# Optimization experiments

Hardware: AMD Instinct MI355X
Metric: run time of the kernel (lower is better)

## Reference

```python
import jax, jax.numpy as jnp
import numpy as np

QC = 12          # effective quantum channels (quantum_channels//4*4)
G = 3            # number of 4-channel quantum groups
DIM = 128
NGROUPS_GN = 8
NUM_LAYER = 1

# PauliZ sign table: wire 0 is the most-significant qubit (PennyLane default.qubit)
_SIGNS = np.array([[1.0 - 2.0 * ((k >> (3 - w)) & 1) for w in range(4)]
                   for k in range(16)], dtype=np.float32)


def _apply_rx(state, phi, w):
    # state: [B,2,2,2,2] complex64; phi: [B]; RX = cos(p/2) I - i sin(p/2) X
    c = jnp.cos(0.5 * phi).astype(jnp.complex64)
    s = (-1j) * jnp.sin(0.5 * phi).astype(jnp.complex64)
    U = jnp.stack([jnp.stack([c, s], -1), jnp.stack([s, c], -1)], -2)  # [B,2,2]
    st = jnp.moveaxis(state, 1 + w, -1)
    st = jnp.einsum('bij,b...j->b...i', U, st)
    return jnp.moveaxis(st, -1, 1 + w)


def _apply_cnot(state, c, t):
    st = jnp.moveaxis(state, (1 + c, 1 + t), (-2, -1))
    st = jnp.concatenate([st[..., 0:1, :], st[..., 1:2, ::-1]], axis=-2)
    return jnp.moveaxis(st, (-2, -1), (1 + c, 1 + t))


def _circuit(x4, theta):
    # AngleEmbedding(RX) + NUM_LAYER x Basic_ansatz; x4: [B,4], theta: [4*NUM_LAYER]
    B = x4.shape[0]
    state = jnp.zeros((B, 2, 2, 2, 2), jnp.complex64).at[:, 0, 0, 0, 0].set(1.0)
    for w in range(4):
        state = _apply_rx(state, x4[:, w], w)
    for l in range(NUM_LAYER):
        th = theta[4 * l:4 * (l + 1)]
        for w in range(4):
            state = _apply_rx(state, jnp.broadcast_to(th[w], (B,)), w)
        for c in range(3):
            state = _apply_cnot(state, c, c + 1)
        state = _apply_cnot(state, 3, 0)
    probs = jnp.abs(state.reshape(B, 16)) ** 2
    return probs @ jnp.asarray(_SIGNS)  # [B,4] PauliZ expvals


def _quantum_block(x_q, qparams):
    # x_q: [B,H,W,QC]; pool spatially, run per-group circuit, broadcast back
    B, H, W, Cq = x_q.shape
    pooled = jnp.mean(x_q, axis=(1, 2)).reshape(B, Cq // 4, 4)
    y = jax.vmap(_circuit, in_axes=(1, 0), out_axes=1)(pooled, qparams)  # [B,G,4]
    y = y.reshape(B, 1, 1, Cq)
    return jnp.broadcast_to(y, (B, H, W, Cq))


def _ws_conv(x, kernel, bias):
    eps = 1e-5  # fp32 branch of WeightStandardizedConv
    mean = jnp.mean(kernel, axis=(0, 1, 2), keepdims=True)
    var = jnp.var(kernel, axis=(0, 1, 2), keepdims=True)
    k = (kernel - mean) / jnp.sqrt(var + eps)
    y = jax.lax.conv_general_dilated(x, k, (1, 1), ((1, 1), (1, 1)),
                                     dimension_numbers=('NHWC', 'HWIO', 'NHWC'))
    return y + bias


def _group_norm(x, scale, bias, groups=NGROUPS_GN, eps=1e-6):
    B, H, W, C = x.shape
    xg = x.reshape(B, H, W, groups, C // groups)
    mu = jnp.mean(xg, axis=(1, 2, 4), keepdims=True)
    var = jnp.var(xg, axis=(1, 2, 4), keepdims=True)
    xn = ((xg - mu) / jnp.sqrt(var + eps)).reshape(B, H, W, C)
    return xn * scale + bias


def setup_inputs() -> dict:
    key = jax.random.key(0)
    ks = jax.random.split(key, 8)
    B, H, W, C, T = 16, 64, 64, DIM, 512
    cc = DIM - QC  # classical conv channels = 116
    return {
        'x': jax.random.normal(ks[0], (B, H, W, C), jnp.float32),
        'time_emb': jax.random.normal(ks[1], (B, T), jnp.float32),
        'qparams': jax.random.uniform(ks[2], (G, 4), jnp.float32),
        'conv0_kernel': jax.random.normal(ks[3], (3, 3, cc, cc), jnp.float32) * 0.05,
        'conv0_bias': jnp.zeros((cc,), jnp.float32),
        'conv1_kernel': jax.random.normal(ks[4], (3, 3, cc, cc), jnp.float32) * 0.05,
        'conv1_bias': jnp.zeros((cc,), jnp.float32),
        'gn0_scale': jnp.ones((C,), jnp.float32),
        'gn0_bias': jnp.zeros((C,), jnp.float32),
        'gn1_scale': jnp.ones((C,), jnp.float32),
        'gn1_bias': jnp.zeros((C,), jnp.float32),
        'time_w': jax.random.normal(ks[5], (T, 2 * DIM), jnp.float32) * 0.02,
        'time_b': jnp.zeros((2 * DIM,), jnp.float32),
    }


def reference(x, time_emb, qparams, conv0_kernel, conv0_bias, conv1_kernel,
              conv1_bias, gn0_scale, gn0_bias, gn1_scale, gn1_bias, time_w, time_b):
    # first quantum + classical branch
    h_q = _quantum_block(x[..., :QC], qparams)
    h_c = _ws_conv(x[..., QC:], conv0_kernel, conv0_bias)
    h = jnp.concatenate([h_q, h_c], axis=-1)
    h = _group_norm(h, gn0_scale, gn0_bias)
    # FiLM conditioning from time embedding
    t = jax.nn.swish(time_emb) @ time_w + time_b  # [B, 2*DIM]
    scale, shift = jnp.split(t[:, None, None, :], 2, axis=-1)
    h = jax.nn.swish(h * (1 + scale) + shift)
    # second quantum + classical branch
    h_q2 = _quantum_block(h[..., :QC], qparams)
    h_c2 = _ws_conv(h[..., QC:], conv1_kernel, conv1_bias)
    h2 = jnp.concatenate([h_q2, h_c2], axis=-1)
    h2 = jax.nn.swish(_group_norm(h2, gn1_scale, gn1_bias))
    return x + h2
```

## Files before the change

### kernel.cpp

```cpp
#include <hip/hip_runtime.h>
#include <math.h>

#define BATCH 16
#define NPX 4096
#define CDIM 128
#define CC 116
#define KTAPS 1044

using u16 = unsigned short;
typedef __attribute__((ext_vector_type(8))) short short8;
typedef __attribute__((ext_vector_type(16))) float f32x16;

__device__ __forceinline__ float swishf(float z) {
    return z / (1.f + __expf(-z));
}
__device__ __forceinline__ float bf2f(u16 u) {
    union { unsigned int i; float f; } v; v.i = ((unsigned int)u) << 16; return v.f;
}
__device__ __forceinline__ u16 f2bf(float f) {
    union { float f; unsigned int i; } v; v.f = f;
    unsigned int r = v.i + 0x7fffu + ((v.i >> 16) & 1u);
    return (u16)(r >> 16);
}

__global__ void k_pre(const float* __restrict__ x, float* __restrict__ part,
                      float* __restrict__ csums) {
    const int bx = blockIdx.x, tid = threadIdx.x;
    if (bx >= 128) {
        int i = (bx - 128) * 256 + tid;
        csums[i * 2] = 0.f;
        csums[i * 2 + 1] = 0.f;
        return;
    }
    const int b = bx >> 3, seg = bx & 7;
    float s[12];
#pragma unroll
    for (int c = 0; c < 12; ++c) s[c] = 0.f;
    const float* xb = x + (size_t)(b * 4096 + seg * 512) * CDIM;
#pragma unroll
    for (int i = 0; i < 2; ++i) {
        const float4* p = (const float4*)(xb + (size_t)(tid + i * 256) * CDIM);
        float4 v0 = p[0], v1 = p[1], v2 = p[2];
        s[0] += v0.x; s[1] += v0.y; s[2] += v0.z; s[3] += v0.w;
        s[4] += v1.x; s[5] += v1.y; s[6] += v1.z; s[7] += v1.w;
        s[8] += v2.x; s[9] += v2.y; s[10] += v2.z; s[11] += v2.w;
    }
    __shared__ float red[12][256];
#pragma unroll
    for (int c = 0; c < 12; ++c) red[c][tid] = s[c];
    __syncthreads();
    for (int st = 128; st > 0; st >>= 1) {
        if (tid < st) {
#pragma unroll
            for (int c = 0; c < 12; ++c) red[c][tid] += red[c][tid + st];
        }
        __syncthreads();
    }
    if (tid < 12) part[bx * 12 + tid] = red[tid][0];
}

__device__ void run_circuit(const float* ang, const float* th, float* z) {
    float ar[16], ai[16];
#pragma unroll
    for (int k = 0; k < 16; ++k) { ar[k] = 0.f; ai[k] = 0.f; }
    ar[0] = 1.f;
#pragma unroll
    for (int pass = 0; pass < 2; ++pass) {
        const float* a = pass ? th : ang;
#pragma unroll
        for (int w = 0; w < 4; ++w) {
            float half = 0.5f * a[w];
            float cth = cosf(half), sth = sinf(half);
            int m = 1 << (3 - w);
#pragma unroll
            for (int k = 0; k < 16; ++k) {
                if (k & m) continue;
                int k2 = k | m;
                float r0 = ar[k], i0 = ai[k], r1 = ar[k2], i1 = ai[k2];
                ar[k]  = cth * r0 + sth * i1;
                ai[k]  = cth * i0 - sth * r1;
                ar[k2] = sth * i0 + cth * r1;
                ai[k2] = -sth * r0 + cth * i1;
            }
        }
    }
#pragma unroll
    for (int e = 0; e < 4; ++e) {
        const int cwi[4] = {0, 1, 2, 3};
        const int twi[4] = {1, 2, 3, 0};
        int mc = 1 << (3 - cwi[e]), mt = 1 << (3 - twi[e]);
#pragma unroll
        for (int k = 0; k < 16; ++k) {
            if ((k & mc) && !(k & mt)) {
                int k2 = k | mt;
                float tr = ar[k]; ar[k] = ar[k2]; ar[k2] = tr;
                float ti = ai[k]; ai[k] = ai[k2]; ai[k2] = ti;
            }
        }
    }
    float zz[4] = {0.f, 0.f, 0.f, 0.f};
#pragma unroll
    for (int k = 0; k < 16; ++k) {
        float p = ar[k] * ar[k] + ai[k] * ai[k];
#pragma unroll
        for (int w = 0; w < 4; ++w) zz[w] += ((k >> (3 - w)) & 1) ? -p : p;
    }
#pragma unroll
    for (int w = 0; w < 4; ++w) z[w] = zz[w];
}

__global__ void k_tw(const float* __restrict__ te, const float* __restrict__ W,
                     const float* __restrict__ tb, float* __restrict__ t,
                     const float* __restrict__ K0, const float* __restrict__ K1,
                     u16* __restrict__ kqp0, u16* __restrict__ kqp1) {
    const int bx = blockIdx.x, tid = threadIdx.x;
    __shared__ float se[512];
    __shared__ float rs[256], rss[256], mb[2];
    if (bx < 16) {
        const int b = bx;
        for (int k = tid; k < 512; k += 256) se[k] = swishf(te[b * 512 + k]);
        __syncthreads();
        float acc = tb[tid];
        for (int k = 0; k < 512; ++k) acc += se[k] * W[k * 256 + tid];
        t[b * 256 + tid] = acc;
        return;
    }
    const int r = bx - 16;
    const float* K = (r >> 7) ? K1 : K0;
    u16* kqp = (r >> 7) ? kqp1 : kqp0;
    const int o = r & 127;
    float s = 0.f, ss = 0.f;
    if (o < CC) {
        for (int idx = tid; idx < KTAPS; idx += 256) {
            float v = K[(size_t)idx * CC + o];
            s += v; ss += v * v;
        }
    }
    rs[tid] = s; rss[tid] = ss;
    __syncthreads();
    for (int st = 128; st > 0; st >>= 1) {
        if (tid < st) { rs[tid] += rs[tid + st]; rss[tid] += rss[tid + st]; }
        __syncthreads();
    }
    if (tid == 0) {
        float m = rs[0] * (1.f / KTAPS);
        float var = rss[0] * (1.f / KTAPS) - m * m;
        mb[0] = m;
        mb[1] = rsqrtf(var + 1e-5f);
    }
    __syncthreads();
    float m = mb[0], inv = mb[1];
    for (int idx = tid; idx < 1152; idx += 256) {
        int tap = idx >> 7, ic = idx & 127;
        float v = 0.f;
        if (o < CC && ic < CC) v = (K[((size_t)tap * CC + ic) * CC + o] - m) * inv;
        int step = tap * 8 + (ic >> 4);
        int lane2 = ((ic >> 3) & 1) * 32 + (o & 31);
        int j = ic & 7;
        kqp[(size_t)(step * 4 + (o >> 5)) * 512 + lane2 * 8 + j] = f2bf(v);
    }
}

template <int MODE>
__launch_bounds__(512, 4)
__global__ void k_conv(const void* __restrict__ inp, const float* __restrict__ Acoef,
                       const float* __restrict__ Bcoef, const u16* __restrict__ kqp,
                       const float* __restrict__ bias, u16* __restrict__ outp,
                       float* __restrict__ csum) {
    __shared__ u16 As[32768];
    __shared__ float cf[256];
    const int hb = blockIdx.x, b = blockIdx.y;
    const int hp = ((hb & 7) << 2) | (hb >> 3);
    const int h0 = hp * 2;
    const int tid = threadIdx.x, lane = tid & 63, wid = tid >> 6;
    const int wm = wid & 1, wn = wid >> 1;
    const int l31 = lane & 31;
    const int rr = tid >> 8, pp = (tid >> 2) & 63, ck = tid & 3;
    const int swz = (pp & 15) << 4;

    if (MODE == 1) {
        if (tid < 128) {
            cf[tid] = Acoef[b * 128 + tid];
            cf[128 + tid] = Bcoef[b * 128 + tid];
        }
    }

    float fv[32]; short8 sv[4];

#define LOADCHUNK(r, val) do { \
    const int hi_ = h0 + (r) - 1; \
    val = (hi_ >= 0 && hi_ < 64); \
    if (val) { \
        const size_t px_ = (size_t)((b * 64 + hi_) * 64 + pp); \
        if (MODE == 0) { \
            const float* sp_ = (const float*)inp + px_ * 128 + 12 + ck * 32; \
            if (ck < 3) { \
                _Pragma("unroll") for (int j = 0; j < 8; ++j) *(float4*)&fv[j * 4] = ((const float4*)sp_)[j]; \
            } else { \
                _Pragma("unroll") for (int j = 0; j < 5; ++j) *(float4*)&fv[j * 4] = ((const float4*)sp_)[j]; \
                _Pragma("unroll") for (int e = 20; e < 32; ++e) fv[e] = 0.f; \
            } \
        } else { \
            const u16* sp_ = (const u16*)inp + px_ * 128 + ck * 32; \
            _Pragma("unroll") for (int k = 0; k < 4; ++k) sv[k] = ((const short8*)sp_)[k]; \
        } \
    } \
} while (0)

#define WRITECHUNK(r, val) do { \
    u16 t_[32]; \
    if (val) { \
        if (MODE == 0) { \
            _Pragma("unroll") for (int e = 0; e < 32; ++e) t_[e] = f2bf(fv[e]); \
        } else { \
            _Pragma("unroll") for (int e = 0; e < 32; ++e) { \
                int c_ = ck * 32 + e; \
                if (c_ < CC) { \
                    float f_ = bf2f((u16)sv[e >> 3][e & 7]); \
                    t_[e] = f2bf(swishf(f_ * cf[12 + c_] + cf[140 + c_])); \
                } else t_[e] = 0; \
            } \
        } \
    } else { \
        _Pragma("unroll") for (int e = 0; e < 32; ++e) t_[e] = 0; \
    } \
    char* rb_ = (char*)As + ((r) * 64 + pp) * 256; \
    _Pragma("unroll") for (int k = 0; k < 4; ++k) \
        *(short8*)(rb_ + ((ck * 64 + k * 16) ^ swz)) = *(const short8*)&t_[k * 8]; \
} while (0)

    bool valA, valC;
    LOADCHUNK(rr, valA);
    if (MODE == 1) __syncthreads();
    WRITECHUNK(rr, valA);
    LOADCHUNK(2 + rr, valC);

    const u16* bp = kqp + (size_t)wn * 512 + (size_t)lane * 8;
    short8 breg[4];
#pragma unroll
    for (int s = 0; s < 4; ++s) breg[s] = *(const short8*)(bp + ((size_t)s << 11));

    const int kh16 = (lane >> 5) << 4;
    int coloff[2][3], colswz[2][3];
#pragma unroll
    for (int mf = 0; mf < 2; ++mf)
#pragma unroll
        for (int q = 0; q < 3; ++q) {
            int c = mf * 32 + l31 + q - 1;
            int cc = c < 0 ? 0 : (c > 63 ? 63 : c);
            coloff[mf][q] = cc << 7;
            colswz[mf][q] = (cc & 15) << 4;
        }
    const bool e0 = (l31 == 0), e1 = (l31 == 31);
    const short8 zero8 = {0, 0, 0, 0, 0, 0, 0, 0};
    const int rowb = wm * 8192;

    asm volatile("s_waitcnt lgkmcnt(0)" ::: "memory");
    __builtin_amdgcn_s_barrier();

    f32x16 acc[2];
#pragma unroll
    for (int mf = 0; mf < 2; ++mf)
#pragma unroll
        for (int r = 0; r < 16; ++r) acc[mf][r] = 0.f;

#define AREAD(dst, s) do { \
    const int tap_ = (s) >> 3, p_ = tap_ / 3, q_ = tap_ % 3; \
    const int chb_ = ((s) & 7) << 5; \
    dst[0] = *(const short8*)&As[rowb + p_ * 8192 + coloff[0][q_] + (((chb_ + kh16) ^ colswz[0][q_]) >> 1)]; \
    dst[1] = *(const short8*)&As[rowb + p_ * 8192 + coloff[1][q_] + (((chb_ + kh16) ^ colswz[1][q_]) >> 1)]; \
} while (0)

#define STEP(s, base, lim) do { \
    const int cur_ = ((s) - (base)) & 1, nxt_ = cur_ ^ 1; \
    if ((s) + 1 < (lim)) AREAD(afr[nxt_], (s) + 1); \
    const int q_ = ((s) >> 3) % 3; \
    short8 a0_ = afr[cur_][0], a1_ = afr[cur_][1]; \
    if (q_ == 0) a0_ = e0 ? zero8 : a0_; \
    if (q_ == 2) a1_ = e1 ? zero8 : a1_; \
    acc[0] = __builtin_amdgcn_mfma_f32_32x32x16_bf16(a0_, breg[(s) & 3], acc[0], 0, 0, 0); \
    acc[1] = __builtin_amdgcn_mfma_f32_32x32x16_bf16(a1_, breg[(s) & 3], acc[1], 0, 0, 0); \
    if ((s) + 4 < 72) breg[(s) & 3] = *(const short8*)(bp + ((size_t)((s) + 4) << 11)); \
} while (0)

    short8 afr[2][2];
    AREAD(afr[0], 0);
#pragma unroll
    for (int s = 0; s < 24; ++s) STEP(s, 0, 24);

    WRITECHUNK(2 + rr, valC);
    asm volatile("s_waitcnt lgkmcnt(0)" ::: "memory");
    __builtin_amdgcn_s_barrier();

    AREAD(afr[0], 24);
#pragma unroll
    for (int s = 24; s < 72; ++s) STEP(s, 24, 72);

    const int oc = wn * 32 + l31;
    const float bv = (oc < CC) ? bias[oc] : 0.f;
    float cs = 0.f, cq = 0.f;
    const int rbase = (lane >> 5) << 2;

    asm volatile("s_waitcnt lgkmcnt(0)" ::: "memory");
    __builtin_amdgcn_s_barrier();
#pragma unroll
    for (int mf = 0; mf < 2; ++mf) {
#pragma unroll
        for (int r = 0; r < 16; ++r) {
            int drow = (r & 3) + ((r >> 2) << 3) + rbase;
            int flat = wm * 64 + mf * 32 + drow;
            float v = acc[mf][r] + bv;
            As[flat * 128 + oc] = f2bf(v);
            cs += v;
            cq += v * v;
        }
    }
    asm volatile("s_waitcnt lgkmcnt(0)" ::: "memory");
    __builtin_amdgcn_s_barrier();
    {
        size_t obase = (size_t)(b * 4096 + h0 * 64) * 128;
#pragma unroll
        for (int k = 0; k < 4; ++k)
            *(short8*)&outp[obase + k * 4096 + tid * 8] = *(const short8*)&As[k * 4096 + tid * 8];
    }
    cs += __shfl_xor(cs, 32);
    cq += __shfl_xor(cq, 32);
    if (lane < 32) {
        atomicAdd(&csum[(b * 128 + oc) * 2], cs);
        atomicAdd(&csum[(b * 128 + oc) * 2 + 1], cq);
    }
#undef LOADCHUNK
#undef WRITECHUNK
#undef AREAD
#undef STEP
}

__global__ void k_mid0(const float* __restrict__ part, const float* __restrict__ csum,
                       const float* __restrict__ t, const float* __restrict__ gs,
                       const float* __restrict__ gb, const float* __restrict__ qp,
                       float* __restrict__ A, float* __restrict__ Bc,
                       float* __restrict__ y2) {
    __shared__ float pooled_s[192], y1s[192], sst[128][2];
    int tid = threadIdx.x;
    if (tid < 192) {
        int b = tid / 12, c = tid % 12;
        float s = 0.f;
#pragma unroll
        for (int k = 0; k < 8; ++k) s += part[(b * 8 + k) * 12 + c];
        pooled_s[tid] = s * (1.f / 4096.f);
    }
    __syncthreads();
    if (tid < 48) {
        int b = tid / 3, g = tid % 3;
        float z[4];
        run_circuit(&pooled_s[b * 12 + g * 4], qp + g * 4, z);
#pragma unroll
        for (int w = 0; w < 4; ++w) y1s[b * 12 + g * 4 + w] = z[w];
    }
    __syncthreads();
    if (tid < 128) {
        int b = tid >> 3, g = tid & 7;
        float S = 0.f, SS = 0.f;
#pragma unroll
        for (int e = 0; e < 16; ++e) {
            int orig = g * 16 + e;
            if (orig >= 12) {
                int cc = orig - 12;
                S += csum[(b * 128 + cc) * 2];
                SS += csum[(b * 128 + cc) * 2 + 1];
            }
        }
        if (g == 0) {
#pragma unroll
            for (int c = 0; c < 12; ++c) {
                float v = y1s[b * 12 + c];
                S += 4096.f * v;
                SS += 4096.f * v * v;
            }
        }
        float mu = S * (1.f / 65536.f);
        float var = SS * (1.f / 65536.f) - mu * mu;
        sst[tid][0] = mu;
        sst[tid][1] = rsqrtf(var + 1e-6f);
    }
    __syncthreads();
    for (int i = tid; i < 2048; i += 256) {
        int b = i >> 7, c = i & 127, g = c >> 4;
        float mu = sst[b * 8 + g][0], isd = sst[b * 8 + g][1];
        float sc = t[b * 256 + c], sh = t[b * 256 + 128 + c];
        float a = isd * gs[c];
        float bb = gb[c] - mu * a;
        A[i] = a * (1.f + sc);
        Bc[i] = bb * (1.f + sc) + sh;
    }
    if (tid < 48) {
        int b = tid / 3, gq = tid % 3;
        float pin[4], z[4];
        float mu = sst[b * 8][0], isd = sst[b * 8][1];
#pragma unroll
        for (int w = 0; w < 4; ++w) {
            int c = gq * 4 + w;
            float a = isd * gs[c];
            float bb = gb[c] - mu * a;
            float sc = t[b * 256 + c], sh = t[b * 256 + 128 + c];
            float v = y1s[b * 12 + c];
            pin[w] = swishf(v * (a * (1.f + sc)) + (bb * (1.f + sc) + sh));
        }
        run_circuit(pin, qp + gq * 4, z);
#pragma unroll
        for (int w = 0; w < 4; ++w) y2[b * 12 + gq * 4 + w] = z[w];
    }
}

__global__ void k_mid1(const float* __restrict__ csum, const float* __restrict__ y2,
                       const float* __restrict__ gs, const float* __restrict__ gb,
                       float* __restrict__ A2, float* __restrict__ B2,
                       float* __restrict__ oq) {
    __shared__ float sst[128][2];
    int tid = threadIdx.x;
    if (tid < 128) {
        int b = tid >> 3, g = tid & 7;
        float S = 0.f, SS = 0.f;
#pragma unroll
        for (int e = 0; e < 16; ++e) {
            int orig = g * 16 + e;
            if (orig >= 12) {
                int cc = orig - 12;
                S += csum[(b * 128 + cc) * 2];
                SS += csum[(b * 128 + cc) * 2 + 1];
            }
        }
        if (g == 0) {
#pragma unroll
            for (int c = 0; c < 12; ++c) {
                float v = y2[b * 12 + c];
                S += 4096.f * v;
                SS += 4096.f * v * v;
            }
        }
        float mu = S * (1.f / 65536.f);
        float var = SS * (1.f / 65536.f) - mu * mu;
        sst[tid][0] = mu;
        sst[tid][1] = rsqrtf(var + 1e-6f);
    }
    __syncthreads();
    for (int i = tid; i < 2048; i += 256) {
        int b = i >> 7, c = i & 127, g = c >> 4;
        float mu = sst[b * 8 + g][0], isd = sst[b * 8 + g][1];
        float a = isd * gs[c];
        A2[i] = a;
        B2[i] = gb[c] - mu * a;
    }
    if (tid < 192) {
        int b = tid / 12, c = tid % 12;
        float mu = sst[b * 8][0], isd = sst[b * 8][1];
        float a = isd * gs[c];
        float bb = gb[c] - mu * a;
        oq[b * 12 + c] = swishf(y2[b * 12 + c] * a + bb);
    }
}

__global__ void k_final(const float* __restrict__ x, const u16* __restrict__ co,
                        const float* __restrict__ A2, const float* __restrict__ B2,
                        const float* __restrict__ oq, float* __restrict__ outp) {
    const int t = blockIdx.x, b = blockIdx.y;
    const int seg = t >> 6, hraw = t & 63;
    const int h = ((hraw & 7) << 3) | (hraw >> 3);
    const int tid = threadIdx.x;
    const size_t px = (size_t)(b * 64 + h) * 64 + seg * 8 + (tid >> 5);
    const int c4 = tid & 31, c = c4 * 4;
    float4 xv = *(const float4*)(x + px * CDIM + c);
    float4 r;
    if (c4 < 3) {
        const float* q = oq + b * 12 + c;
        r.x = xv.x + q[0]; r.y = xv.y + q[1]; r.z = xv.z + q[2]; r.w = xv.w + q[3];
    } else {
        int cc = c - 12;
        const u16* hp = co + px * 128 + cc;
        float4 a = *(const float4*)(A2 + b * 128 + c);
        float4 bb = *(const float4*)(B2 + b * 128 + c);
        r.x = xv.x + swishf(bf2f(hp[0]) * a.x + bb.x);
        r.y = xv.y + swishf(bf2f(hp[1]) * a.y + bb.y);
        r.z = xv.z + swishf(bf2f(hp[2]) * a.z + bb.z);
        r.w = xv.w + swishf(bf2f(hp[3]) * a.w + bb.w);
    }
    *(float4*)(outp + px * CDIM + c) = r;
}

extern "C" void kernel_launch(void* const* d_in, const int* in_sizes, int n_in,
                              void* d_out, int out_size, void* d_ws, size_t ws_size,
                              hipStream_t stream) {
    const float* x        = (const float*)d_in[0];
    const float* time_emb = (const float*)d_in[1];
    const float* qparams  = (const float*)d_in[2];
    const float* c0k      = (const float*)d_in[3];
    const float* c0b      = (const float*)d_in[4];
    const float* c1k      = (const float*)d_in[5];
    const float* c1b      = (const float*)d_in[6];
    const float* g0s      = (const float*)d_in[7];
    const float* g0b      = (const float*)d_in[8];
    const float* g1s      = (const float*)d_in[9];
    const float* g1b      = (const float*)d_in[10];
    const float* tw       = (const float*)d_in[11];
    const float* tb       = (const float*)d_in[12];
    float* outp = (float*)d_out;
    float* ws = (float*)d_ws;

    size_t o = 0;
    auto alloc = [&](size_t n) { size_t r = o; o += (n + 15) & ~(size_t)15; return r; };
    float* part   = ws + alloc(1536);
    float* csums  = ws + alloc(8192);
    float* csum0  = csums;
    float* csum1  = csums + 4096;
    float* t      = ws + alloc(4096);
    float* A      = ws + alloc(2048);
    float* Bc     = ws + alloc(2048);
    float* A2     = ws + alloc(2048);
    float* B2     = ws + alloc(2048);
    float* y2     = ws + alloc(192);
    float* oq     = ws + alloc(192);
    u16* kqp0     = (u16*)(ws + alloc(73728));
    u16* kqp1     = (u16*)(ws + alloc(73728));
    u16* convA    = (u16*)(ws + alloc(4194304));
    u16* convB    = (u16*)(ws + alloc(4194304));

    k_pre<<<144, 256, 0, stream>>>(x, part, csums);
    k_tw<<<272, 256, 0, stream>>>(time_emb, tw, tb, t, c0k, c1k, kqp0, kqp1);

    dim3 cgrid(32, 16);
    k_conv<0><<<cgrid, 512, 0, stream>>>(x, nullptr, nullptr, kqp0, c0b, convA, csum0);
    k_mid0<<<1, 256, 0, stream>>>(part, csum0, t, g0s, g0b, qparams, A, Bc, y2);

    k_conv<1><<<cgrid, 512, 0, stream>>>(convA, A, Bc, kqp1, c1b, convB, csum1);
    k_mid1<<<1, 256, 0, stream>>>(csum1, y2, g1s, g1b, A2, B2, oq);
    k_final<<<dim3(512, 16), 256, 0, stream>>>(x, convB, A2, B2, oq, outp);
}
```

Before: 127.2 us.

## Deepen conv MFMA operand prefetch, add setprio and sched barriers, pad coef LDS

```diff
diff --git a/kernel.cpp b/kernel.cpp
--- a/kernel.cpp
+++ b/kernel.cpp
@@ -168,7 +168,7 @@
                        const float* __restrict__ bias, u16* __restrict__ outp,
                        float* __restrict__ csum) {
     __shared__ u16 As[32768];
-    __shared__ float cf[256];
+    __shared__ float cfA[132], cfB[132];
     const int hb = blockIdx.x, b = blockIdx.y;
     const int hp = ((hb & 7) << 2) | (hb >> 3);
     const int h0 = hp * 2;
@@ -180,8 +180,14 @@
 
     if (MODE == 1) {
         if (tid < 128) {
-            cf[tid] = Acoef[b * 128 + tid];
-            cf[128 + tid] = Bcoef[b * 128 + tid];
+            int ckk = tid >> 5, ee = tid & 31;
+            float a = 0.f, bbv = 0.f;
+            if (tid < CC) {
+                a = Acoef[b * 128 + 12 + tid];
+                bbv = Bcoef[b * 128 + 12 + tid];
+            }
+            cfA[ckk * 33 + ee] = a;
+            cfB[ckk * 33 + ee] = bbv;
         }
     }
 
@@ -215,10 +221,9 @@
         } else { \
             _Pragma("unroll") for (int e = 0; e < 32; ++e) { \
                 int c_ = ck * 32 + e; \
-                if (c_ < CC) { \
-                    float f_ = bf2f((u16)sv[e >> 3][e & 7]); \
-                    t_[e] = f2bf(swishf(f_ * cf[12 + c_] + cf[140 + c_])); \
-                } else t_[e] = 0; \
+                float f_ = bf2f((u16)sv[e >> 3][e & 7]); \
+                float w_ = swishf(f_ * cfA[ck * 33 + e] + cfB[ck * 33 + e]); \
+                t_[e] = (c_ < CC) ? f2bf(w_) : (u16)0; \
             } \
         } \
     } else { \
@@ -236,9 +241,9 @@
     LOADCHUNK(2 + rr, valC);
 
     const u16* bp = kqp + (size_t)wn * 512 + (size_t)lane * 8;
-    short8 breg[4];
-#pragma unroll
-    for (int s = 0; s < 4; ++s) breg[s] = *(const short8*)(bp + ((size_t)s << 11));
+    short8 breg[5];
+#pragma unroll
+    for (int s = 0; s < 5; ++s) breg[s] = *(const short8*)(bp + ((size_t)s << 11));
 
     const int kh16 = (lane >> 5) << 4;
     int coloff[2][3], colswz[2][3];
@@ -256,6 +261,7 @@
     const int rowb = wm * 8192;
 
     asm volatile("s_waitcnt lgkmcnt(0)" ::: "memory");
+    __builtin_amdgcn_sched_barrier(0);
     __builtin_amdgcn_s_barrier();
 
     f32x16 acc[2];
@@ -272,27 +278,32 @@
 } while (0)
 
 #define STEP(s, base, lim) do { \
-    const int cur_ = ((s) - (base)) & 1, nxt_ = cur_ ^ 1; \
-    if ((s) + 1 < (lim)) AREAD(afr[nxt_], (s) + 1); \
+    const int cur_ = ((s) - (base)) % 3; \
+    if ((s) + 2 < (lim)) AREAD(afr[((s) - (base) + 2) % 3], (s) + 2); \
     const int q_ = ((s) >> 3) % 3; \
     short8 a0_ = afr[cur_][0], a1_ = afr[cur_][1]; \
     if (q_ == 0) a0_ = e0 ? zero8 : a0_; \
     if (q_ == 2) a1_ = e1 ? zero8 : a1_; \
-    acc[0] = __builtin_amdgcn_mfma_f32_32x32x16_bf16(a0_, breg[(s) & 3], acc[0], 0, 0, 0); \
-    acc[1] = __builtin_amdgcn_mfma_f32_32x32x16_bf16(a1_, breg[(s) & 3], acc[1], 0, 0, 0); \
-    if ((s) + 4 < 72) breg[(s) & 3] = *(const short8*)(bp + ((size_t)((s) + 4) << 11)); \
+    __builtin_amdgcn_s_setprio(1); \
+    acc[0] = __builtin_amdgcn_mfma_f32_32x32x16_bf16(a0_, breg[(s) % 5], acc[0], 0, 0, 0); \
+    acc[1] = __builtin_amdgcn_mfma_f32_32x32x16_bf16(a1_, breg[(s) % 5], acc[1], 0, 0, 0); \
+    __builtin_amdgcn_s_setprio(0); \
+    if ((s) + 5 < 72) breg[((s) + 5) % 5] = *(const short8*)(bp + ((size_t)((s) + 5) << 11)); \
 } while (0)
 
-    short8 afr[2][2];
+    short8 afr[3][2];
     AREAD(afr[0], 0);
+    AREAD(afr[1], 1);
 #pragma unroll
     for (int s = 0; s < 24; ++s) STEP(s, 0, 24);
 
     WRITECHUNK(2 + rr, valC);
     asm volatile("s_waitcnt lgkmcnt(0)" ::: "memory");
+    __builtin_amdgcn_sched_barrier(0);
     __builtin_amdgcn_s_barrier();
 
     AREAD(afr[0], 24);
+    AREAD(afr[1], 25);
 #pragma unroll
     for (int s = 24; s < 72; ++s) STEP(s, 24, 72);
 
@@ -302,6 +313,7 @@
     const int rbase = (lane >> 5) << 2;
 
     asm volatile("s_waitcnt lgkmcnt(0)" ::: "memory");
+    __builtin_amdgcn_sched_barrier(0);
     __builtin_amdgcn_s_barrier();
 #pragma unroll
     for (int mf = 0; mf < 2; ++mf) {
@@ -316,6 +328,7 @@
         }
     }
     asm volatile("s_waitcnt lgkmcnt(0)" ::: "memory");
+    __builtin_amdgcn_sched_barrier(0);
     __builtin_amdgcn_s_barrier();
     {
         size_t obase = (size_t)(b * 4096 + h0 * 64) * 128;
```

Result: slower. 136.4 us (+7.3%).
